# Kernel tuning notes

Hardware: AMD Instinct MI355X
Metric: run time of the kernel (lower is better)

The kernel has to match this reference:

```python
import jax, jax.numpy as jnp
import numpy as np

N_DIALOGS = 60
DIA_LEN = 100
N = N_DIALOGS * DIA_LEN  # 6000 utterances total
D_IN = 512
D_OUT = 512


def setup_inputs() -> dict:
    key = jax.random.key(0)
    k1, k2, k3, k4 = jax.random.split(key, 4)
    inputs = jax.random.normal(k1, (N, D_IN), dtype=jnp.float32)
    # per-dialog lengths (concrete host array; defines static graph structure)
    dia_len = np.full((N_DIALOGS,), DIA_LEN, dtype=np.int64)
    # one-hot speaker mask [N, 1, 2]; qmask[j,0,0]==1 -> speaker0 else speaker1
    sp = jax.random.randint(k2, (N,), 0, 2)
    qmask = jnp.zeros((N, 1, 2), jnp.int64).at[jnp.arange(N), 0, sp].set(1)
    W = jax.random.normal(k3, (D_OUT, D_IN), dtype=jnp.float32) / np.sqrt(D_IN)
    b = jax.random.normal(k4, (D_OUT,), dtype=jnp.float32) * 0.01
    return {"inputs": inputs, "dia_len": dia_len, "qmask": qmask, "W": W, "b": b}


def build_adj(inputs, dia_len, qmask):
    # Vectorized equivalent of message_passing_directed_speaker:
    # adj = I; edge (i,j) iff i,j in same dialog, same speaker, and consecutive
    # among that speaker's utterances; weight = 1 - arccos(clip(cos,-1,1))/pi.
    n = inputs.shape[0]
    dia_len_np = np.asarray(dia_len)
    did = jnp.asarray(np.repeat(np.arange(len(dia_len_np)), dia_len_np))  # dialog id per node
    sp0 = qmask[:, 0, 0] == 1  # True -> speaker0
    cs0 = jnp.cumsum(sp0.astype(jnp.int32))
    cs1 = jnp.cumsum((~sp0).astype(jnp.int32))
    csel = jnp.where(sp0, cs0, cs1)  # running count of own speaker
    idx = jnp.arange(n)
    # j>i, same dialog, same speaker, no same-speaker utterance strictly between
    upper = ((did[None, :] == did[:, None])
             & (sp0[None, :] == sp0[:, None])
             & (csel[None, :] - csel[:, None] == 1)
             & (idx[None, :] > idx[:, None]))
    edge = upper | upper.T
    # pairwise cosine similarity (cossim returns 0 when a norm is 0)
    nrm = jnp.sqrt(jnp.sum(inputs * inputs, axis=-1))  # [N]
    denom = nrm[:, None] * nrm[None, :]
    dots = inputs @ inputs.T  # [N, N]
    cos = jnp.where(denom > 0, dots / jnp.where(denom > 0, denom, 1.0), 0.0)
    cos_safe = jnp.where(edge, jnp.clip(cos, -1.0, 1.0), 0.0)
    w = 1.0 - jnp.arccos(cos_safe) / jnp.pi
    return jnp.where(edge, w, 0.0) + jnp.eye(n, dtype=inputs.dtype)


def reference(inputs, dia_len, qmask, W, b):
    adj = build_adj(inputs, dia_len, qmask)  # [N, N]
    x = adj @ inputs                          # [N, D_IN]
    return x @ W.T + b                        # [N, D_OUT]
```

## Files before the change

### kernel.cpp

```cpp
#include <hip/hip_runtime.h>
#include <hip/hip_bf16.h>

#define N_NODES 6000
#define N_DIA   60
#define DIA     100
#define DDIM    512
#define LDA     520

typedef short short8   __attribute__((ext_vector_type(8)));
typedef float floatx4  __attribute__((ext_vector_type(4)));

__device__ __forceinline__ unsigned short f2bf(float f) {
    unsigned int u = __float_as_uint(f);
    unsigned int r = (u + 0x7fffu + ((u >> 16) & 1u)) >> 16;
    return (unsigned short)r;
}

__device__ __forceinline__ float wave_reduce_sum(float v) {
    #pragma unroll
    for (int off = 32; off > 0; off >>= 1) v += __shfl_xor(v, off, 64);
    return v;
}

__global__ __launch_bounds__(256) void wcast_kernel(
    const float* __restrict__ W, unsigned short* __restrict__ wbf)
{
    int base = blockIdx.x * 2048 + threadIdx.x * 8;
    float4 a = *(const float4*)(W + base);
    float4 b = *(const float4*)(W + base + 4);
    union { unsigned short u[8]; short8 v; } o;
    o.u[0]=f2bf(a.x); o.u[1]=f2bf(a.y); o.u[2]=f2bf(a.z); o.u[3]=f2bf(a.w);
    o.u[4]=f2bf(b.x); o.u[5]=f2bf(b.y); o.u[6]=f2bf(b.z); o.u[7]=f2bf(b.w);
    *(short8*)(wbf + base) = o.v;
}

__global__ __launch_bounds__(512, 4) void fused_kernel(
    const float* __restrict__ x, const int* __restrict__ qmask,
    const unsigned short* __restrict__ wbf, const float* __restrict__ bias,
    float* __restrict__ out)
{
    __shared__ unsigned short As[32 * LDA];
    int tid = threadIdx.x;
    int wv = tid >> 6, lane = tid & 63;
    int m0 = blockIdx.x * 32;

    int cached_d = -1;
    unsigned long long sm_a = 0, sm_b = 0;
    #pragma unroll
    for (int t = 0; t < 4; ++t) {
        int rr = wv * 4 + t;
        int i = m0 + rr;
        unsigned short* dst = As + rr * LDA + lane * 8;
        if (i >= N_NODES) {
            *(short8*)dst = (short8)0;
            continue;
        }
        int d = i / DIA;
        int dstart = d * DIA;
        if (d != cached_d) {
            sm_a = __ballot(qmask[2 * (dstart + lane)] == 1);
            sm_b = __ballot(lane < 36 && qmask[2 * (dstart + 64 + lane)] == 1);
            cached_d = d;
        }
        int pos = i - dstart;
        int sp = (pos < 64) ? (int)((sm_a >> pos) & 1)
                            : (int)((sm_b >> (pos - 64)) & 1);
        unsigned long long Ma = sp ? sm_a : ~sm_a;
        unsigned long long Mb = sp ? sm_b : (~sm_b & 0xFFFFFFFFFULL);

        int j = -1;
        {
            unsigned long long aa = (pos < 64) ? (Ma & ~((2ULL << pos) - 1)) : 0ULL;
            if (aa) j = dstart + __builtin_ctzll(aa);
            else {
                unsigned long long bb = (pos >= 64)
                    ? (Mb & ~((2ULL << (pos - 64)) - 1)) : Mb;
                if (bb) j = dstart + 64 + __builtin_ctzll(bb);
            }
        }
        int p = -1;
        {
            unsigned long long bb = (pos > 64)
                ? (Mb & ((1ULL << (pos - 64)) - 1)) : 0ULL;
            if (bb) p = dstart + 64 + (63 - __builtin_clzll(bb));
            else {
                unsigned long long aa = (pos >= 64) ? Ma
                    : (pos ? (Ma & ((1ULL << pos) - 1)) : 0ULL);
                if (aa) p = dstart + (63 - __builtin_clzll(aa));
            }
        }

        const float* ri = x + (size_t)i * DDIM + lane * 8;
        float4 ia = *(const float4*)(ri);
        float4 ib = *(const float4*)(ri + 4);
        float ni = ia.x*ia.x + ia.y*ia.y + ia.z*ia.z + ia.w*ia.w
                 + ib.x*ib.x + ib.y*ib.y + ib.z*ib.z + ib.w*ib.w;
        float4 ja, jb; float dij = 0.0f, nj = 0.0f;
        if (j >= 0) {
            const float* rj = x + (size_t)j * DDIM + lane * 8;
            ja = *(const float4*)(rj);
            jb = *(const float4*)(rj + 4);
            dij = ia.x*ja.x + ia.y*ja.y + ia.z*ja.z + ia.w*ja.w
                + ib.x*jb.x + ib.y*jb.y + ib.z*jb.z + ib.w*jb.w;
            nj  = ja.x*ja.x + ja.y*ja.y + ja.z*ja.z + ja.w*ja.w
                + jb.x*jb.x + jb.y*jb.y + jb.z*jb.z + jb.w*jb.w;
        }
        float4 pa, pb; float dpi = 0.0f, np_ = 0.0f;
        if (p >= 0) {
            const float* rp = x + (size_t)p * DDIM + lane * 8;
            pa = *(const float4*)(rp);
            pb = *(const float4*)(rp + 4);
            dpi = ia.x*pa.x + ia.y*pa.y + ia.z*pa.z + ia.w*pa.w
                + ib.x*pb.x + ib.y*pb.y + ib.z*pb.z + ib.w*pb.w;
            np_ = pa.x*pa.x + pa.y*pa.y + pa.z*pa.z + pa.w*pa.w
                + pb.x*pb.x + pb.y*pb.y + pb.z*pb.z + pb.w*pb.w;
        }
        ni = wave_reduce_sum(ni);
        float wj = 0.0f, wp = 0.0f;
        if (j >= 0) {
            dij = wave_reduce_sum(dij);
            nj  = wave_reduce_sum(nj);
            float dn = ni * nj;
            float c = (dn > 0.0f) ? (dij * __frsqrt_rn(dn)) : 0.0f;
            c = fminf(1.0f, fmaxf(-1.0f, c));
            wj = 1.0f - acosf(c) * 0.3183098861837907f;
        }
        if (p >= 0) {
            dpi = wave_reduce_sum(dpi);
            np_ = wave_reduce_sum(np_);
            float dn = ni * np_;
            float c = (dn > 0.0f) ? (dpi * __frsqrt_rn(dn)) : 0.0f;
            c = fminf(1.0f, fmaxf(-1.0f, c));
            wp = 1.0f - acosf(c) * 0.3183098861837907f;
        }

        float acc[8];
        acc[0]=ia.x; acc[1]=ia.y; acc[2]=ia.z; acc[3]=ia.w;
        acc[4]=ib.x; acc[5]=ib.y; acc[6]=ib.z; acc[7]=ib.w;
        if (j >= 0) {
            acc[0]+=wj*ja.x; acc[1]+=wj*ja.y; acc[2]+=wj*ja.z; acc[3]+=wj*ja.w;
            acc[4]+=wj*jb.x; acc[5]+=wj*jb.y; acc[6]+=wj*jb.z; acc[7]+=wj*jb.w;
        }
        if (p >= 0) {
            acc[0]+=wp*pa.x; acc[1]+=wp*pa.y; acc[2]+=wp*pa.z; acc[3]+=wp*pa.w;
            acc[4]+=wp*pb.x; acc[5]+=wp*pb.y; acc[6]+=wp*pb.z; acc[7]+=wp*pb.w;
        }
        union { unsigned short u[8]; short8 v; } o;
        #pragma unroll
        for (int q = 0; q < 8; ++q) o.u[q] = f2bf(acc[q]);
        *(short8*)dst = o.v;
    }
    __syncthreads();

    int n0 = blockIdx.y * 256 + wv * 32;
    int fr = lane & 15;
    int kq = (lane >> 4) * 8;
    floatx4 acc2[2][2] = {};
    const unsigned short* As_base = As + fr * LDA + kq;
    const unsigned short* bb = wbf + (size_t)(n0 + fr) * DDIM + kq;

    #pragma unroll 4
    for (int k = 0; k < DDIM; k += 32) {
        short8 af[2], bfv[2];
        af[0] = *(const short8*)(As_base + k);
        af[1] = *(const short8*)(As_base + 16 * LDA + k);
        bfv[0] = *(const short8*)(bb + k);
        bfv[1] = *(const short8*)(bb + (size_t)16 * DDIM + k);
        #pragma unroll
        for (int ms = 0; ms < 2; ++ms)
            #pragma unroll
            for (int ns = 0; ns < 2; ++ns)
                acc2[ms][ns] = __builtin_amdgcn_mfma_f32_16x16x32_bf16(
                    af[ms], bfv[ns], acc2[ms][ns], 0, 0, 0);
    }

    int col = lane & 15;
    int rbase = (lane >> 4) * 4;
    #pragma unroll
    for (int ns = 0; ns < 2; ++ns) {
        int n = n0 + ns * 16 + col;
        float bv = bias[n];
        #pragma unroll
        for (int ms = 0; ms < 2; ++ms) {
            #pragma unroll
            for (int r = 0; r < 4; ++r) {
                int m = m0 + ms * 16 + rbase + r;
                if (m < N_NODES)
                    out[(size_t)m * DDIM + n] = acc2[ms][ns][r] + bv;
            }
        }
    }
}

extern "C" void kernel_launch(void* const* d_in, const int* in_sizes, int n_in,
                              void* d_out, int out_size, void* d_ws, size_t ws_size,
                              hipStream_t stream) {
    const float* inputs = (const float*)d_in[0];
    const int* qmask   = (const int*)d_in[2];
    const float* W     = (const float*)d_in[3];
    const float* bias  = (const float*)d_in[4];
    float* out = (float*)d_out;

    unsigned short* wbf = (unsigned short*)d_ws;

    wcast_kernel<<<128, 256, 0, stream>>>(W, wbf);
    fused_kernel<<<dim3(188, 2), 512, 0, stream>>>(inputs, qmask, wbf, bias, out);
}
```

Before: 98.42 us.

## Shrink M tile to 16 rows and drop N split to avoid redundant aggregation

Each block now aggregates 16 rows and computes all 512 output columns, instead of 32 rows split across two blocks in the column dimension. The old scheme repeated the graph aggregation and cosine computation in both column blocks. The new grid is 375 blocks with no bounds checks, since 6000 divides by 16. Each wave now does a 16x64 MFMA tile, loading four B fragments per k step, so there is less A reuse per B load. Loads are also restructured to stay inside the branches, and the row loop is no longer unrolled.

```diff
diff --git a/kernel.cpp b/kernel.cpp
--- a/kernel.cpp
+++ b/kernel.cpp
@@ -1,11 +1,11 @@
 #include <hip/hip_runtime.h>
-#include <hip/hip_bf16.h>
 
 #define N_NODES 6000
 #define N_DIA   60
 #define DIA     100
 #define DDIM    512
 #define LDA     520
+#define TILE_M  16
 
 typedef short short8   __attribute__((ext_vector_type(8)));
 typedef float floatx4  __attribute__((ext_vector_type(4)));
@@ -39,22 +39,17 @@
     const unsigned short* __restrict__ wbf, const float* __restrict__ bias,
     float* __restrict__ out)
 {
-    __shared__ unsigned short As[32 * LDA];
+    __shared__ unsigned short As[TILE_M * LDA];
     int tid = threadIdx.x;
     int wv = tid >> 6, lane = tid & 63;
-    int m0 = blockIdx.x * 32;
+    int m0 = blockIdx.x * TILE_M;
 
     int cached_d = -1;
     unsigned long long sm_a = 0, sm_b = 0;
-    #pragma unroll
-    for (int t = 0; t < 4; ++t) {
-        int rr = wv * 4 + t;
+    #pragma unroll 1
+    for (int t = 0; t < 2; ++t) {
+        int rr = wv * 2 + t;
         int i = m0 + rr;
-        unsigned short* dst = As + rr * LDA + lane * 8;
-        if (i >= N_NODES) {
-            *(short8*)dst = (short8)0;
-            continue;
-        }
         int d = i / DIA;
         int dstart = d * DIA;
         if (d != cached_d) {
@@ -95,100 +90,81 @@
         float4 ib = *(const float4*)(ri + 4);
         float ni = ia.x*ia.x + ia.y*ia.y + ia.z*ia.z + ia.w*ia.w
                  + ib.x*ib.x + ib.y*ib.y + ib.z*ib.z + ib.w*ib.w;
-        float4 ja, jb; float dij = 0.0f, nj = 0.0f;
+        ni = wave_reduce_sum(ni);
+
+        float acc[8];
+        acc[0]=ia.x; acc[1]=ia.y; acc[2]=ia.z; acc[3]=ia.w;
+        acc[4]=ib.x; acc[5]=ib.y; acc[6]=ib.z; acc[7]=ib.w;
+
         if (j >= 0) {
             const float* rj = x + (size_t)j * DDIM + lane * 8;
-            ja = *(const float4*)(rj);
-            jb = *(const float4*)(rj + 4);
-            dij = ia.x*ja.x + ia.y*ja.y + ia.z*ja.z + ia.w*ja.w
-                + ib.x*jb.x + ib.y*jb.y + ib.z*jb.z + ib.w*jb.w;
-            nj  = ja.x*ja.x + ja.y*ja.y + ja.z*ja.z + ja.w*ja.w
-                + jb.x*jb.x + jb.y*jb.y + jb.z*jb.z + jb.w*jb.w;
-        }
-        float4 pa, pb; float dpi = 0.0f, np_ = 0.0f;
-        if (p >= 0) {
-            const float* rp = x + (size_t)p * DDIM + lane * 8;
-            pa = *(const float4*)(rp);
-            pb = *(const float4*)(rp + 4);
-            dpi = ia.x*pa.x + ia.y*pa.y + ia.z*pa.z + ia.w*pa.w
-                + ib.x*pb.x + ib.y*pb.y + ib.z*pb.z + ib.w*pb.w;
-            np_ = pa.x*pa.x + pa.y*pa.y + pa.z*pa.z + pa.w*pa.w
-                + pb.x*pb.x + pb.y*pb.y + pb.z*pb.z + pb.w*pb.w;
-        }
-        ni = wave_reduce_sum(ni);
-        float wj = 0.0f, wp = 0.0f;
-        if (j >= 0) {
+            float4 ja = *(const float4*)(rj);
+            float4 jb = *(const float4*)(rj + 4);
+            float dij = ia.x*ja.x + ia.y*ja.y + ia.z*ja.z + ia.w*ja.w
+                      + ib.x*jb.x + ib.y*jb.y + ib.z*jb.z + ib.w*jb.w;
+            float nj  = ja.x*ja.x + ja.y*ja.y + ja.z*ja.z + ja.w*ja.w
+                      + jb.x*jb.x + jb.y*jb.y + jb.z*jb.z + jb.w*jb.w;
             dij = wave_reduce_sum(dij);
             nj  = wave_reduce_sum(nj);
             float dn = ni * nj;
             float c = (dn > 0.0f) ? (dij * __frsqrt_rn(dn)) : 0.0f;
             c = fminf(1.0f, fmaxf(-1.0f, c));
-            wj = 1.0f - acosf(c) * 0.3183098861837907f;
+            float wj = 1.0f - acosf(c) * 0.3183098861837907f;
+            acc[0]+=wj*ja.x; acc[1]+=wj*ja.y; acc[2]+=wj*ja.z; acc[3]+=wj*ja.w;
+            acc[4]+=wj*jb.x; acc[5]+=wj*jb.y; acc[6]+=wj*jb.z; acc[7]+=wj*jb.w;
         }
         if (p >= 0) {
+            const float* rp = x + (size_t)p * DDIM + lane * 8;
+            float4 pa = *(const float4*)(rp);
+            float4 pb = *(const float4*)(rp + 4);
+            float dpi = ia.x*pa.x + ia.y*pa.y + ia.z*pa.z + ia.w*pa.w
+                      + ib.x*pb.x + ib.y*pb.y + ib.z*pb.z + ib.w*pb.w;
+            float np_ = pa.x*pa.x + pa.y*pa.y + pa.z*pa.z + pa.w*pa.w
+                      + pb.x*pb.x + pb.y*pb.y + pb.z*pb.z + pb.w*pb.w;
             dpi = wave_reduce_sum(dpi);
             np_ = wave_reduce_sum(np_);
             float dn = ni * np_;
             float c = (dn > 0.0f) ? (dpi * __frsqrt_rn(dn)) : 0.0f;
             c = fminf(1.0f, fmaxf(-1.0f, c));
-            wp = 1.0f - acosf(c) * 0.3183098861837907f;
-        }
-
-        float acc[8];
-        acc[0]=ia.x; acc[1]=ia.y; acc[2]=ia.z; acc[3]=ia.w;
-        acc[4]=ib.x; acc[5]=ib.y; acc[6]=ib.z; acc[7]=ib.w;
-        if (j >= 0) {
-            acc[0]+=wj*ja.x; acc[1]+=wj*ja.y; acc[2]+=wj*ja.z; acc[3]+=wj*ja.w;
-            acc[4]+=wj*jb.x; acc[5]+=wj*jb.y; acc[6]+=wj*jb.z; acc[7]+=wj*jb.w;
-        }
-        if (p >= 0) {
+            float wp = 1.0f - acosf(c) * 0.3183098861837907f;
             acc[0]+=wp*pa.x; acc[1]+=wp*pa.y; acc[2]+=wp*pa.z; acc[3]+=wp*pa.w;
             acc[4]+=wp*pb.x; acc[5]+=wp*pb.y; acc[6]+=wp*pb.z; acc[7]+=wp*pb.w;
         }
+
         union { unsigned short u[8]; short8 v; } o;
         #pragma unroll
         for (int q = 0; q < 8; ++q) o.u[q] = f2bf(acc[q]);
-        *(short8*)dst = o.v;
+        *(short8*)(As + rr * LDA + lane * 8) = o.v;
     }
     __syncthreads();
 
-    int n0 = blockIdx.y * 256 + wv * 32;
+    int n0 = wv * 64;
     int fr = lane & 15;
     int kq = (lane >> 4) * 8;
-    floatx4 acc2[2][2] = {};
+    floatx4 acc2[4] = {};
     const unsigned short* As_base = As + fr * LDA + kq;
     const unsigned short* bb = wbf + (size_t)(n0 + fr) * DDIM + kq;
 
     #pragma unroll 4
     for (int k = 0; k < DDIM; k += 32) {
-        short8 af[2], bfv[2];
-        af[0] = *(const short8*)(As_base + k);
-        af[1] = *(const short8*)(As_base + 16 * LDA + k);
-        bfv[0] = *(const short8*)(bb + k);
-        bfv[1] = *(const short8*)(bb + (size_t)16 * DDIM + k);
+        short8 af = *(const short8*)(As_base + k);
         #pragma unroll
-        for (int ms = 0; ms < 2; ++ms)
-            #pragma unroll
-            for (int ns = 0; ns < 2; ++ns)
-                acc2[ms][ns] = __builtin_amdgcn_mfma_f32_16x16x32_bf16(
-                    af[ms], bfv[ns], acc2[ms][ns], 0, 0, 0);
+        for (int ns = 0; ns < 4; ++ns) {
+            short8 bv = *(const short8*)(bb + (size_t)ns * 16 * DDIM + k);
+            acc2[ns] = __builtin_amdgcn_mfma_f32_16x16x32_bf16(
+                af, bv, acc2[ns], 0, 0, 0);
+        }
     }
 
     int col = lane & 15;
     int rbase = (lane >> 4) * 4;
     #pragma unroll
-    for (int ns = 0; ns < 2; ++ns) {
+    for (int ns = 0; ns < 4; ++ns) {
         int n = n0 + ns * 16 + col;
         float bv = bias[n];
         #pragma unroll
-        for (int ms = 0; ms < 2; ++ms) {
-            #pragma unroll
-            for (int r = 0; r < 4; ++r) {
-                int m = m0 + ms * 16 + rbase + r;
-                if (m < N_NODES)
-                    out[(size_t)m * DDIM + n] = acc2[ms][ns][r] + bv;
-            }
-        }
+        for (int r = 0; r < 4; ++r)
+            out[(size_t)(m0 + rbase + r) * DDIM + n] = acc2[ns][r] + bv;
     }
 }
 
@@ -204,5 +180,5 @@
     unsigned short* wbf = (unsigned short*)d_ws;
 
     wcast_kernel<<<128, 256, 0, stream>>>(W, wbf);
-    fused_kernel<<<dim3(188, 2), 512, 0, stream>>>(inputs, qmask, wbf, bias, out);
+    fused_kernel<<<N_NODES / TILE_M, 512, 0, stream>>>(inputs, qmask, wbf, bias, out);
 }
```

New measurement: 104.9 us. 1.07x slower.
